# Performance work log

Hardware: AMD Instinct MI355X
Metric: run time of the kernel (lower is better)

## Reference

```python
import jax, jax.numpy as jnp
import numpy as np
from jax import lax

B, C, T, F = 8, 96, 1000, 64
L = 12          # n_layers
K = 3           # band_kernel_size (odd)
EPS = 1e-6


def _rms(x, w):
    # x: (B,C,F); RMSNorm over channel dim with learned per-channel scale
    return x * lax.rsqrt(jnp.mean(x * x, axis=1, keepdims=True) + EPS) * w[None, :, None]


def _dwconv(x, w, b):
    # depthwise conv along freq axis; x: (B,C,F), w: (C,1,K)
    y = lax.conv_general_dilated(
        x, w, window_strides=(1,), padding=[(K // 2, K // 2)],
        dimension_numbers=('NCH', 'OIH', 'NCH'), feature_group_count=C)
    return y + b[None, :, None]


def _cell(y, hp, inw, hnw, xw, xb, hw, hb, pw, pb, onw):
    # one ConvGRUBandCell2d frame step; y, hp: (B,C,F)
    xg = jnp.einsum('oc,bcf->bof', xw, _rms(y, inw)) + xb[None, :, None]
    hg = jnp.einsum('oc,bcf->bof', pw, _dwconv(_rms(hp, hnw), hw, hb)) + pb[None, :, None]
    xr, xz, xn = jnp.split(xg, 3, axis=1)
    hr, hz, hn = jnp.split(hg, 3, axis=1)
    reset = jax.nn.sigmoid(xr + hr)
    update = jax.nn.sigmoid(xz + hz)
    cand = jnp.tanh(xn + reset * hn)
    h_new = (1.0 - update) * cand + update * hp
    return _rms(h_new + y, onw)  # out_norm(h_new + x_t); this is also the stored state


def setup_inputs() -> dict:
    key = jax.random.key(0)
    ks = jax.random.split(key, 7)
    s = 0.05
    return {
        'x': jax.random.normal(ks[0], (B, C, T, F), dtype=jnp.float32),
        'in_norm_w': jnp.ones((L, C), jnp.float32),
        'hid_norm_w': jnp.ones((L, C), jnp.float32),
        'xproj_w': jax.random.normal(ks[1], (L, 3 * C, C), jnp.float32) * s,
        'xproj_b': jax.random.normal(ks[2], (L, 3 * C), jnp.float32) * s,
        'hmix_w': jax.random.normal(ks[3], (L, C, 1, K), jnp.float32) * s,
        'hmix_b': jax.random.normal(ks[4], (L, C), jnp.float32) * s,
        'hproj_w': jax.random.normal(ks[5], (L, 3 * C, C), jnp.float32) * s,
        'hproj_b': jax.random.normal(ks[6], (L, 3 * C), jnp.float32) * s,
        'out_norm_w': jnp.ones((L, C), jnp.float32),
    }


def reference(x, in_norm_w, hid_norm_w, xproj_w, xproj_b, hmix_w, hmix_b,
              hproj_w, hproj_b, out_norm_w):
    # x: (B,C,T,F) -> (B,C,T,F)
    h0 = jnp.zeros((L, x.shape[0], C, x.shape[-1]), x.dtype)
    params = (in_norm_w, hid_norm_w, xproj_w, xproj_b, hmix_w, hmix_b,
              hproj_w, hproj_b, out_norm_w)

    def time_step(h_all, x_t):          # h_all: (L,B,C,F), x_t: (B,C,F)
        def layer_step(y, xs):
            hp = xs[0]
            out = _cell(y, hp, *xs[1:])
            return out, out
        y, h_new = lax.scan(layer_step, x_t, (h_all,) + params)
        return h_new, y

    _, ys = lax.scan(time_step, h0, jnp.moveaxis(x, 2, 0))  # ys: (T,B,C,F)
    return jnp.moveaxis(ys, 0, 2)
```

## Files before the change

### kernel.cpp

```cpp
#include <hip/hip_runtime.h>

#define BB 8
#define CC 96
#define TT 1000
#define FF 64
#define LL 12

__device__ __forceinline__ float sigmoidf_(float v) {
    return 1.0f / (1.0f + __expf(-v));
}

union SmemU {
    float hp[CC][35];
    float w[2][288][12];
};

__global__ __launch_bounds__(256) void cell_diag(
    const float* __restrict__ x,
    const float* __restrict__ inw_all,
    const float* __restrict__ hnw_all,
    const float* __restrict__ xw_all,
    const float* __restrict__ xb_all,
    const float* __restrict__ hw_all,
    const float* __restrict__ hb_all,
    const float* __restrict__ pw_all,
    const float* __restrict__ pb_all,
    const float* __restrict__ onw_all,
    float* __restrict__ out,
    float* __restrict__ H,
    int d, int l_start)
{
    const int cell = blockIdx.x >> 4;
    const int sub  = blockIdx.x & 15;
    const int l = l_start + cell;
    const int t = d - l;
    const int b = sub >> 1;
    const int f0 = (sub & 1) << 5;

    __shared__ __align__(16) float ybuf[CC][36];
    __shared__ __align__(16) float hnb[CC][36];
    __shared__ __align__(16) SmemU su;
    __shared__ float s_y[32];
    __shared__ float s_h[34];

    const int tid = threadIdx.x;

    const float* inw = inw_all + l*CC;
    const float* hnw = hnw_all + l*CC;
    const float* xw  = xw_all + (size_t)l*288*CC;
    const float* xb  = xb_all + l*288;
    const float* hw  = hw_all + l*CC*3;
    const float* hb  = hb_all + l*CC;
    const float* pw  = pw_all + (size_t)l*288*CC;
    const float* pb  = pb_all + l*288;
    const float* onw = onw_all + l*CC;

    const int bufW = d & 1;
    const int bufR = (d + 1) & 1;

    const float* ysrc;
    int ystride;
    if (l == 0) { ysrc = x + (size_t)b*CC*TT*FF + (size_t)t*FF + f0; ystride = TT*FF; }
    else        { ysrc = H + ((((size_t)bufR*LL + (l-1))*BB + b)*CC)*FF + f0; ystride = FF; }

    #pragma unroll
    for (int i = 0; i < 12; i++) {
        int idx = i*256 + tid;
        int c = idx >> 5, j = idx & 31;
        ybuf[c][j] = ysrc[(size_t)c*ystride + j];
    }

    const float* hpsrc = H + ((((size_t)bufR*LL + l)*BB + b)*CC)*FF;
    for (int idx = tid; idx < CC*34; idx += 256) {
        int c = idx / 34, jh = idx % 34;
        int f = f0 - 1 + jh;
        float v = 0.0f;
        if (t > 0 && f >= 0 && f < FF) v = hpsrc[c*FF + f];
        su.hp[c][jh] = v;
    }
    __syncthreads();

    if (tid < 32) {
        float s = 0.0f;
        for (int c = 0; c < CC; c++) { float v = ybuf[c][tid]; s += v*v; }
        s_y[tid] = rsqrtf(s * (1.0f/CC) + 1e-6f);
    } else if (tid >= 64 && tid < 98) {
        int jh = tid - 64;
        float s = 0.0f;
        for (int c = 0; c < CC; c++) { float v = su.hp[c][jh]; s += v*v; }
        s_h[jh] = rsqrtf(s * (1.0f/CC) + 1e-6f);
    }
    __syncthreads();

    #pragma unroll
    for (int i = 0; i < 12; i++) {
        int idx = i*256 + tid;
        int c = idx >> 5, j = idx & 31;
        float w0 = hw[c*3+0], w1 = hw[c*3+1], w2 = hw[c*3+2];
        float p0 = su.hp[c][j]   * s_h[j];
        float p1 = su.hp[c][j+1] * s_h[j+1];
        float p2 = su.hp[c][j+2] * s_h[j+2];
        hnb[c][j] = (w0*p0 + w1*p1 + w2*p2) * hnw[c] + hb[c];
    }
    __syncthreads();

    const int tx = tid & 7, ty = tid >> 3;
    const int j0 = tx << 2;
    float accx[3][3][4];
    float accp[3][3][4];
    #pragma unroll
    for (int a = 0; a < 3; a++)
        #pragma unroll
        for (int g = 0; g < 3; g++)
            #pragma unroll
            for (int m = 0; m < 4; m++) { accx[a][g][m] = 0.0f; accp[a][g][m] = 0.0f; }

    float syj[4];
    #pragma unroll
    for (int m = 0; m < 4; m++) syj[m] = s_y[j0 + m];

    for (int cc8 = 0; cc8 < 12; cc8++) {
        int c0 = cc8 * 8;
        #pragma unroll
        for (int i = 0; i < 9; i++) {
            int idx = i*256 + tid;
            int o = idx >> 3, ci = idx & 7;
            su.w[0][o][ci] = xw[(size_t)o*CC + c0 + ci];
            su.w[1][o][ci] = pw[(size_t)o*CC + c0 + ci];
        }
        __syncthreads();
        #pragma unroll
        for (int c4 = 0; c4 < 2; c4++) {
            int cl = c4 * 4;
            int cg = c0 + cl;
            float ya[4][4], ha[4][4];
            #pragma unroll
            for (int k = 0; k < 4; k++) {
                const float4 yv = *(const float4*)&ybuf[cg + k][j0];
                const float4 hv = *(const float4*)&hnb[cg + k][j0];
                float sc = inw[cg + k];
                ya[k][0] = yv.x * syj[0] * sc;
                ya[k][1] = yv.y * syj[1] * sc;
                ya[k][2] = yv.z * syj[2] * sc;
                ya[k][3] = yv.w * syj[3] * sc;
                ha[k][0] = hv.x; ha[k][1] = hv.y; ha[k][2] = hv.z; ha[k][3] = hv.w;
            }
            #pragma unroll
            for (int a = 0; a < 3; a++)
                #pragma unroll
                for (int g = 0; g < 3; g++) {
                    int row = ty + 32*a + 96*g;
                    const float4 wx4 = *(const float4*)&su.w[0][row][cl];
                    const float4 wp4 = *(const float4*)&su.w[1][row][cl];
                    #pragma unroll
                    for (int m = 0; m < 4; m++) {
                        accx[a][g][m] += wx4.x*ya[0][m] + wx4.y*ya[1][m]
                                       + wx4.z*ya[2][m] + wx4.w*ya[3][m];
                        accp[a][g][m] += wp4.x*ha[0][m] + wp4.y*ha[1][m]
                                       + wp4.z*ha[2][m] + wp4.w*ha[3][m];
                    }
                }
        }
        __syncthreads();
    }

    #pragma unroll
    for (int a = 0; a < 3; a++) {
        int co = ty + 32*a;
        float xbr = xb[co], xbz = xb[co+96], xbn = xb[co+192];
        float pbr = pb[co], pbz = pb[co+96], pbn = pb[co+192];
        #pragma unroll
        for (int m = 0; m < 4; m++) {
            int j = j0 + m;
            float r = sigmoidf_(accx[a][0][m] + xbr + accp[a][0][m] + pbr);
            float z = sigmoidf_(accx[a][1][m] + xbz + accp[a][1][m] + pbz);
            float cn = tanhf(accx[a][2][m] + xbn + r * (accp[a][2][m] + pbn));
            float hpv = (t > 0) ? hpsrc[co*FF + f0 + j] : 0.0f;
            float hnew = (1.0f - z) * cn + z * hpv;
            ybuf[co][j] = hnew + ybuf[co][j];
        }
    }
    __syncthreads();

    if (tid < 32) {
        float s = 0.0f;
        for (int c = 0; c < CC; c++) { float v = ybuf[c][tid]; s += v*v; }
        s_y[tid] = rsqrtf(s * (1.0f/CC) + 1e-6f);
    }
    __syncthreads();

    float* hdst = H + ((((size_t)bufW*LL + l)*BB + b)*CC)*FF + f0;
    float* odst = out + (size_t)b*CC*TT*FF + (size_t)t*FF + f0;
    #pragma unroll
    for (int i = 0; i < 12; i++) {
        int idx = i*256 + tid;
        int c = idx >> 5, j = idx & 31;
        float v = ybuf[c][j] * s_y[j] * onw[c];
        hdst[(size_t)c*FF + j] = v;
        if (l == LL-1) odst[(size_t)c*TT*FF + j] = v;
    }
}

extern "C" void kernel_launch(void* const* d_in, const int* in_sizes, int n_in,
                              void* d_out, int out_size, void* d_ws, size_t ws_size,
                              hipStream_t stream) {
    const float* x   = (const float*)d_in[0];
    const float* inw = (const float*)d_in[1];
    const float* hnw = (const float*)d_in[2];
    const float* xw  = (const float*)d_in[3];
    const float* xb  = (const float*)d_in[4];
    const float* hw  = (const float*)d_in[5];
    const float* hb  = (const float*)d_in[6];
    const float* pw  = (const float*)d_in[7];
    const float* pb  = (const float*)d_in[8];
    const float* onw = (const float*)d_in[9];
    float* out = (float*)d_out;
    float* H   = (float*)d_ws;

    for (int d = 0; d < TT + LL - 1; d++) {
        int l_lo = d - (TT - 1); if (l_lo < 0) l_lo = 0;
        int l_hi = d;            if (l_hi > LL - 1) l_hi = LL - 1;
        int nact = l_hi - l_lo + 1;
        cell_diag<<<dim3(nact * 16), dim3(256), 0, stream>>>(
            x, inw, hnw, xw, xb, hw, hb, pw, pb, onw, out, H, d, l_lo);
    }
}
```

Baseline: 47.41 ms.

## Restructure cell kernel: one block per batch, wave-owned channels, weights read directly from global

Each block now covers a full batch row (all 64 freq bins) with 512 threads. Each wave owns 12 output channels per gate and lane maps to frequency. This removes the freq-halo split and the shared-memory weight staging loop with its per-chunk barriers. Weights are read as wave-uniform float4 loads from global/L1, and the RMS reductions use register partial sums plus a small shared reduction. The trade-off is half as many blocks per launch and a heavier per-thread accumulator set (72 floats), which raises register pressure.

Measured after the change: 62.21 ms. 31.2% more time.

```diff
diff --git a/kernel.cpp b/kernel.cpp
--- a/kernel.cpp
+++ b/kernel.cpp
@@ -10,12 +10,8 @@
     return 1.0f / (1.0f + __expf(-v));
 }
 
-union SmemU {
-    float hp[CC][35];
-    float w[2][288][12];
-};
-
-__global__ __launch_bounds__(256) void cell_diag(
+
+__global__ __launch_bounds__(512) void cell_diag(
     const float* __restrict__ x,
     const float* __restrict__ inw_all,
     const float* __restrict__ hnw_all,
@@ -30,20 +26,21 @@
     float* __restrict__ H,
     int d, int l_start)
 {
-    const int cell = blockIdx.x >> 4;
-    const int sub  = blockIdx.x & 15;
+    const int cell = blockIdx.x >> 3;
+    const int b    = blockIdx.x & 7;
     const int l = l_start + cell;
     const int t = d - l;
-    const int b = sub >> 1;
-    const int f0 = (sub & 1) << 5;
-
-    __shared__ __align__(16) float ybuf[CC][36];
-    __shared__ __align__(16) float hnb[CC][36];
-    __shared__ __align__(16) SmemU su;
-    __shared__ float s_y[32];
-    __shared__ float s_h[34];
-
-    const int tid = threadIdx.x;
+
+    const int tid  = threadIdx.x;
+    const int lane = tid & 63;
+    const int wv   = __builtin_amdgcn_readfirstlane(tid >> 6);
+    const int co0  = wv * 12;
+
+    __shared__ float hpn[CC][66];
+    __shared__ float ha[CC][FF];
+    __shared__ float sred[2][8][64];
+    __shared__ float s_y[64];
+    __shared__ float s_h[64];
 
     const float* inw = inw_all + l*CC;
     const float* hnw = hnw_all + l*CC;
@@ -58,146 +55,142 @@
     const int bufW = d & 1;
     const int bufR = (d + 1) & 1;
 
-    const float* ysrc;
-    int ystride;
-    if (l == 0) { ysrc = x + (size_t)b*CC*TT*FF + (size_t)t*FF + f0; ystride = TT*FF; }
-    else        { ysrc = H + ((((size_t)bufR*LL + (l-1))*BB + b)*CC)*FF + f0; ystride = FF; }
-
-    #pragma unroll
-    for (int i = 0; i < 12; i++) {
-        int idx = i*256 + tid;
-        int c = idx >> 5, j = idx & 31;
-        ybuf[c][j] = ysrc[(size_t)c*ystride + j];
-    }
-
+    const float* ysrc; size_t ystride;
+    if (l == 0) { ysrc = x + (size_t)b*CC*TT*FF + (size_t)t*FF; ystride = (size_t)TT*FF; }
+    else        { ysrc = H + ((((size_t)bufR*LL + (l-1))*BB + b)*CC)*FF; ystride = FF; }
     const float* hpsrc = H + ((((size_t)bufR*LL + l)*BB + b)*CC)*FF;
-    for (int idx = tid; idx < CC*34; idx += 256) {
-        int c = idx / 34, jh = idx % 34;
-        int f = f0 - 1 + jh;
-        float v = 0.0f;
-        if (t > 0 && f >= 0 && f < FF) v = hpsrc[c*FF + f];
-        su.hp[c][jh] = v;
-    }
-    __syncthreads();
-
-    if (tid < 32) {
-        float s = 0.0f;
-        for (int c = 0; c < CC; c++) { float v = ybuf[c][tid]; s += v*v; }
+
+    float yreg[12], hreg[12];
+    float ssy = 0.f, ssh = 0.f;
+    #pragma unroll
+    for (int i = 0; i < 12; i++) {
+        const int c = co0 + i;
+        float yv = ysrc[(size_t)c*ystride + lane];
+        float hv = (t > 0) ? hpsrc[(size_t)c*FF + lane] : 0.0f;
+        yreg[i] = yv; hreg[i] = hv;
+        ssy += yv*yv; ssh += hv*hv;
+    }
+    sred[0][wv][lane] = ssy;
+    sred[1][wv][lane] = ssh;
+    __syncthreads();
+
+    if (tid < 64) {
+        float s = 0.f;
+        #pragma unroll
+        for (int w = 0; w < 8; w++) s += sred[0][w][tid];
         s_y[tid] = rsqrtf(s * (1.0f/CC) + 1e-6f);
-    } else if (tid >= 64 && tid < 98) {
-        int jh = tid - 64;
-        float s = 0.0f;
-        for (int c = 0; c < CC; c++) { float v = su.hp[c][jh]; s += v*v; }
-        s_h[jh] = rsqrtf(s * (1.0f/CC) + 1e-6f);
-    }
-    __syncthreads();
-
-    #pragma unroll
-    for (int i = 0; i < 12; i++) {
-        int idx = i*256 + tid;
-        int c = idx >> 5, j = idx & 31;
-        float w0 = hw[c*3+0], w1 = hw[c*3+1], w2 = hw[c*3+2];
-        float p0 = su.hp[c][j]   * s_h[j];
-        float p1 = su.hp[c][j+1] * s_h[j+1];
-        float p2 = su.hp[c][j+2] * s_h[j+2];
-        hnb[c][j] = (w0*p0 + w1*p1 + w2*p2) * hnw[c] + hb[c];
-    }
-    __syncthreads();
-
-    const int tx = tid & 7, ty = tid >> 3;
-    const int j0 = tx << 2;
-    float accx[3][3][4];
-    float accp[3][3][4];
-    #pragma unroll
-    for (int a = 0; a < 3; a++)
-        #pragma unroll
-        for (int g = 0; g < 3; g++)
+    } else if (tid < 128) {
+        const int j = tid - 64;
+        float s = 0.f;
+        #pragma unroll
+        for (int w = 0; w < 8; w++) s += sred[1][w][j];
+        s_h[j] = rsqrtf(s * (1.0f/CC) + 1e-6f);
+    }
+    __syncthreads();
+
+    const float syl = s_y[lane];
+    const float shl = s_h[lane];
+
+    #pragma unroll
+    for (int i = 0; i < 12; i++)
+        hpn[co0+i][1+lane] = hreg[i] * shl;
+    if (lane < 2) {
+        #pragma unroll
+        for (int i = 0; i < 12; i++) hpn[co0+i][lane*65] = 0.f;
+    }
+    __syncthreads();
+
+    #pragma unroll
+    for (int i = 0; i < 12; i++) {
+        const int c = co0 + i;
+        const float w0 = hw[c*3+0], w1 = hw[c*3+1], w2 = hw[c*3+2];
+        ha[c][lane] = (w0*hpn[c][lane] + w1*hpn[c][lane+1] + w2*hpn[c][lane+2])
+                      * hnw[c] + hb[c];
+    }
+    __syncthreads();
+    #pragma unroll
+    for (int i = 0; i < 12; i++) {
+        const int c = co0 + i;
+        hpn[c][lane] = yreg[i] * syl * inw[c];
+    }
+    __syncthreads();
+
+    float accx[3][12], accp[3][12];
+    #pragma unroll
+    for (int g = 0; g < 3; g++)
+        #pragma unroll
+        for (int i = 0; i < 12; i++) { accx[g][i] = 0.f; accp[g][i] = 0.f; }
+
+    #pragma unroll
+    for (int g = 0; g < 3; g++) {
+        const float* xwb = xw + (size_t)(g*CC + co0)*CC;
+        #pragma unroll 4
+        for (int kc = 0; kc < CC; kc += 4) {
+            const float a0 = hpn[kc+0][lane];
+            const float a1 = hpn[kc+1][lane];
+            const float a2 = hpn[kc+2][lane];
+            const float a3 = hpn[kc+3][lane];
             #pragma unroll
-            for (int m = 0; m < 4; m++) { accx[a][g][m] = 0.0f; accp[a][g][m] = 0.0f; }
-
-    float syj[4];
-    #pragma unroll
-    for (int m = 0; m < 4; m++) syj[m] = s_y[j0 + m];
-
-    for (int cc8 = 0; cc8 < 12; cc8++) {
-        int c0 = cc8 * 8;
-        #pragma unroll
-        for (int i = 0; i < 9; i++) {
-            int idx = i*256 + tid;
-            int o = idx >> 3, ci = idx & 7;
-            su.w[0][o][ci] = xw[(size_t)o*CC + c0 + ci];
-            su.w[1][o][ci] = pw[(size_t)o*CC + c0 + ci];
+            for (int i = 0; i < 12; i++) {
+                const float4 w4 = *(const float4*)(xwb + (size_t)i*CC + kc);
+                accx[g][i] += w4.x*a0 + w4.y*a1 + w4.z*a2 + w4.w*a3;
+            }
         }
-        __syncthreads();
-        #pragma unroll
-        for (int c4 = 0; c4 < 2; c4++) {
-            int cl = c4 * 4;
-            int cg = c0 + cl;
-            float ya[4][4], ha[4][4];
+        const float* pwb = pw + (size_t)(g*CC + co0)*CC;
+        #pragma unroll 4
+        for (int kc = 0; kc < CC; kc += 4) {
+            const float a0 = ha[kc+0][lane];
+            const float a1 = ha[kc+1][lane];
+            const float a2 = ha[kc+2][lane];
+            const float a3 = ha[kc+3][lane];
             #pragma unroll
-            for (int k = 0; k < 4; k++) {
-                const float4 yv = *(const float4*)&ybuf[cg + k][j0];
-                const float4 hv = *(const float4*)&hnb[cg + k][j0];
-                float sc = inw[cg + k];
-                ya[k][0] = yv.x * syj[0] * sc;
-                ya[k][1] = yv.y * syj[1] * sc;
-                ya[k][2] = yv.z * syj[2] * sc;
-                ya[k][3] = yv.w * syj[3] * sc;
-                ha[k][0] = hv.x; ha[k][1] = hv.y; ha[k][2] = hv.z; ha[k][3] = hv.w;
+            for (int i = 0; i < 12; i++) {
+                const float4 w4 = *(const float4*)(pwb + (size_t)i*CC + kc);
+                accp[g][i] += w4.x*a0 + w4.y*a1 + w4.z*a2 + w4.w*a3;
             }
-            #pragma unroll
-            for (int a = 0; a < 3; a++)
-                #pragma unroll
-                for (int g = 0; g < 3; g++) {
-                    int row = ty + 32*a + 96*g;
-                    const float4 wx4 = *(const float4*)&su.w[0][row][cl];
-                    const float4 wp4 = *(const float4*)&su.w[1][row][cl];
-                    #pragma unroll
-                    for (int m = 0; m < 4; m++) {
-                        accx[a][g][m] += wx4.x*ya[0][m] + wx4.y*ya[1][m]
-                                       + wx4.z*ya[2][m] + wx4.w*ya[3][m];
-                        accp[a][g][m] += wp4.x*ha[0][m] + wp4.y*ha[1][m]
-                                       + wp4.z*ha[2][m] + wp4.w*ha[3][m];
-                    }
-                }
         }
-        __syncthreads();
-    }
-
-    #pragma unroll
-    for (int a = 0; a < 3; a++) {
-        int co = ty + 32*a;
-        float xbr = xb[co], xbz = xb[co+96], xbn = xb[co+192];
-        float pbr = pb[co], pbz = pb[co+96], pbn = pb[co+192];
-        #pragma unroll
-        for (int m = 0; m < 4; m++) {
-            int j = j0 + m;
-            float r = sigmoidf_(accx[a][0][m] + xbr + accp[a][0][m] + pbr);
-            float z = sigmoidf_(accx[a][1][m] + xbz + accp[a][1][m] + pbz);
-            float cn = tanhf(accx[a][2][m] + xbn + r * (accp[a][2][m] + pbn));
-            float hpv = (t > 0) ? hpsrc[co*FF + f0 + j] : 0.0f;
-            float hnew = (1.0f - z) * cn + z * hpv;
-            ybuf[co][j] = hnew + ybuf[co][j];
+    }
+
+    float v[12];
+    float sso = 0.f;
+    #pragma unroll
+    for (int i = 0; i < 12; i++) {
+        const int c = co0 + i;
+        const float xbr = xb[c], xbz = xb[c+96], xbn = xb[c+192];
+        const float pbr = pb[c], pbz = pb[c+96], pbn = pb[c+192];
+        const float r  = sigmoidf_(accx[0][i] + xbr + accp[0][i] + pbr);
+        const float z  = sigmoidf_(accx[1][i] + xbz + accp[1][i] + pbz);
+        const float cn = tanhf(accx[2][i] + xbn + r * (accp[2][i] + pbn));
+        const float hnew = (1.0f - z) * cn + z * hreg[i];
+        const float vv = hnew + yreg[i];
+        v[i] = vv;
+        sso += vv*vv;
+    }
+    sred[0][wv][lane] = sso;
+    __syncthreads();
+
+    if (tid < 64) {
+        float s = 0.f;
+        #pragma unroll
+        for (int w = 0; w < 8; w++) s += sred[0][w][tid];
+        s_y[tid] = rsqrtf(s * (1.0f/CC) + 1e-6f);
+    }
+    __syncthreads();
+    const float sol = s_y[lane];
+
+    float* hdst = H + ((((size_t)bufW*LL + l)*BB + b)*CC)*FF;
+    #pragma unroll
+    for (int i = 0; i < 12; i++) {
+        const int c = co0 + i;
+        hdst[(size_t)c*FF + lane] = v[i] * sol * onw[c];
+    }
+    if (l == LL-1) {
+        float* odst = out + (size_t)b*CC*TT*FF + (size_t)t*FF;
+        #pragma unroll
+        for (int i = 0; i < 12; i++) {
+            const int c = co0 + i;
+            odst[(size_t)c*TT*FF + lane] = v[i] * sol * onw[c];
         }
-    }
-    __syncthreads();
-
-    if (tid < 32) {
-        float s = 0.0f;
-        for (int c = 0; c < CC; c++) { float v = ybuf[c][tid]; s += v*v; }
-        s_y[tid] = rsqrtf(s * (1.0f/CC) + 1e-6f);
-    }
-    __syncthreads();
-
-    float* hdst = H + ((((size_t)bufW*LL + l)*BB + b)*CC)*FF + f0;
-    float* odst = out + (size_t)b*CC*TT*FF + (size_t)t*FF + f0;
-    #pragma unroll
-    for (int i = 0; i < 12; i++) {
-        int idx = i*256 + tid;
-        int c = idx >> 5, j = idx & 31;
-        float v = ybuf[c][j] * s_y[j] * onw[c];
-        hdst[(size_t)c*FF + j] = v;
-        if (l == LL-1) odst[(size_t)c*TT*FF + j] = v;
     }
 }
 
@@ -221,7 +214,7 @@
         int l_lo = d - (TT - 1); if (l_lo < 0) l_lo = 0;
         int l_hi = d;            if (l_hi > LL - 1) l_hi = LL - 1;
         int nact = l_hi - l_lo + 1;
-        cell_diag<<<dim3(nact * 16), dim3(256), 0, stream>>>(
+        cell_diag<<<dim3(nact * 8), dim3(512), 0, stream>>>(
             x, inw, hnw, xw, xb, hw, hb, pw, pb, onw, out, H, d, l_lo);
     }
 }
```
